# Optimization experiments

Measured on AMD Instinct MI355X. Metric: run time of the kernel, lower is better.

Reference implementation:

```python
import jax, jax.numpy as jnp
import numpy as np

H, C = 3, 64  # heads, per-head channels
NEG_SLOPE = 0.2

def setup_inputs() -> dict:
    key = jax.random.key(0)
    ks = jax.random.split(key, 8)
    B, N, D, E = 2, 50000, 128, 800000
    h = jax.random.normal(ks[0], (B, N, D), dtype=jnp.float32)
    edge_index = jax.random.randint(ks[1], (2, E), 0, N, dtype=jnp.int64)
    s = 1.0 / np.sqrt(D)
    W = jax.random.normal(ks[2], (D, H * C), dtype=jnp.float32) * s
    a_src = jax.random.normal(ks[3], (H, C), dtype=jnp.float32) * (1.0 / np.sqrt(C))
    a_dst = jax.random.normal(ks[4], (H, C), dtype=jnp.float32) * (1.0 / np.sqrt(C))
    bias = jnp.zeros((H * C,), dtype=jnp.float32)
    Wo = jax.random.normal(ks[5], (H * C, 1), dtype=jnp.float32) * (1.0 / np.sqrt(H * C))
    bo = jnp.zeros((1,), dtype=jnp.float32)
    return {"h": h, "edge_index": edge_index, "W": W, "a_src": a_src,
            "a_dst": a_dst, "bias": bias, "Wo": Wo, "bo": bo}

def _gat_single(h_b, src, dst, N, W, a_src, a_dst, bias):
    # h_b: [N, D] -> x: [N, H, C]
    x = (h_b @ W).reshape(-1, H, C)
    alpha_s = jnp.einsum('nhc,hc->nh', x, a_src)  # [N, H]
    alpha_d = jnp.einsum('nhc,hc->nh', x, a_dst)  # [N, H]
    e = alpha_s[src] + alpha_d[dst]               # [E', H]
    e = jnp.where(e > 0, e, NEG_SLOPE * e)        # leaky_relu(0.2)
    # segment softmax over edges grouped by destination node
    emax = jax.ops.segment_max(e, dst, num_segments=N)          # [N, H]
    p = jnp.exp(e - emax[dst])
    denom = jax.ops.segment_sum(p, dst, num_segments=N)         # [N, H]
    att = p / (denom[dst] + 1e-16)                               # [E', H]
    out = jax.ops.segment_sum(att[:, :, None] * x[src], dst, num_segments=N)  # [N,H,C]
    return out.reshape(-1, H * C) + bias

def reference(h, edge_index, W, a_src, a_dst, bias, Wo, bo):
    B, N, D = h.shape
    # PyG GATConv default: add self loops
    loops = jnp.arange(N, dtype=edge_index.dtype)
    src = jnp.concatenate([edge_index[0], loops])
    dst = jnp.concatenate([edge_index[1], loops])
    gat = jax.vmap(lambda hb: _gat_single(hb, src, dst, N, W, a_src, a_dst, bias))(h)
    gat = jax.nn.elu(gat)            # [B, N, H*C]; dropout inactive (eval)
    logits = gat @ Wo + bo           # [B, N, 1]
    return logits
```

## Files before the change

kernel.cpp:

```cpp
#include <hip/hip_runtime.h>
#include <hip/hip_bf16.h>
#include <math.h>

typedef __hip_bfloat16 bf16;
typedef __attribute__((ext_vector_type(8))) short short8;
typedef __attribute__((ext_vector_type(4))) short short4v;
typedef __attribute__((ext_vector_type(4))) float f32x4;

#define HC 192
#define DIN 128
#define NEG_SLOPE 0.2f
#define GN 4
#define CAP 56
#define GROWS 128

static inline int cdiv(int a, int b){ return (a + b - 1) / b; }

__device__ inline short f2bf(float f){
  __hip_bfloat16 b = __float2bfloat16(f);
  return __builtin_bit_cast(short, b);
}
__device__ inline float loadf(const void* p, size_t i, int fm){
  return fm ? __bfloat162float(((const bf16*)p)[i]) : ((const float*)p)[i];
}
__device__ inline int eload(const void* p, long long i, int em){
  return em ? (int)(((const long long*)p)[i]) : ((const int*)p)[i];
}

__device__ inline int detect_fm(const unsigned* __restrict__ hw){
  unsigned w = hw[threadIdx.x & 63];
  unsigned expo = (w >> 7) & 0xFF;
  unsigned long long m = __ballot(expo >= 100 && expo <= 135);
  return __popcll(m) > 32;
}
__device__ inline int detect_em(const unsigned* __restrict__ ew){
  unsigned long long m = __ballot(ew[2*(threadIdx.x & 63) + 1] != 0);
  return __popcll(m) < 32;
}

__global__ void k_repack(const void* __restrict__ W, const void* __restrict__ a_src,
    const void* __restrict__ a_dst, const void* __restrict__ bias,
    const void* __restrict__ Wo, const void* __restrict__ bo,
    const unsigned* __restrict__ hw, bf16* __restrict__ Wt,
    float* __restrict__ asf, float* __restrict__ adf, float* __restrict__ biasf,
    float* __restrict__ Wof, float* __restrict__ bof,
    int* __restrict__ counts, int N){
  int fm = detect_fm(hw);
  int idx = blockIdx.x * 256 + threadIdx.x;
  for (int i = idx; i < N; i += 96 * 256) counts[i] = 0;
  if (idx < DIN * HC){
    int d = idx / HC, j = idx - d * HC;
    Wt[j * DIN + d] = __float2bfloat16(loadf(W, idx, fm));
  }
  if (idx < HC){
    asf[idx]   = loadf(a_src, idx, fm);
    adf[idx]   = loadf(a_dst, idx, fm);
    biasf[idx] = loadf(bias, idx, fm);
    Wof[idx]   = loadf(Wo, idx, fm);
  }
  if (idx == 0) bof[0] = loadf(bo, 0, fm);
}

__global__ __launch_bounds__(512) void k_fused(const void* __restrict__ h,
    const bf16* __restrict__ Wt, bf16* __restrict__ x,
    const float* __restrict__ asf, const float* __restrict__ adf,
    float* __restrict__ asp, float* __restrict__ adp,
    const void* __restrict__ ei, int* __restrict__ counts,
    unsigned* __restrict__ srcs, int M, int N, int E, int NBG){
  __shared__ short ldsW[HC * 136];

  if ((int)blockIdx.x >= NBG){
    int em = detect_em((const unsigned*)ei);
    int idx = ((int)blockIdx.x - NBG) * 512 + (int)threadIdx.x;
    if (idx >= E + N) return;
    int s, d;
    if (idx < E){
      s = eload(ei, idx, em);
      d = eload(ei, (long long)E + idx, em);
    } else { s = d = idx - E; }
    if ((unsigned)d >= (unsigned)N) return;
    if ((unsigned)s >= (unsigned)N) s = 0;
    int slot = atomicAdd(&counts[d], 1);
    if (slot >= CAP) return;
    srcs[(size_t)d * CAP + slot] = (unsigned)s;
    return;
  }

  int fm   = detect_fm((const unsigned*)h);
  int tid  = threadIdx.x;
  int w    = tid >> 6;
  int lane = tid & 63;
  int r16  = lane & 15;
  int quad = lane >> 4;
  for (int c = tid; c < HC * 16; c += 512){
    int row = c >> 4, kg = c & 15;
    *(short8*)&ldsW[row * 136 + kg * 8] = *(const short8*)(Wt + row * DIN + kg * 8);
  }
  __syncthreads();

  int row  = (int)blockIdx.x * GROWS + w * 16 + r16;
  int lrow = min(row, M - 1);
  f32x4 acc[12];
  #pragma unroll
  for (int i = 0; i < 12; i++) acc[i] = (f32x4){0.f,0.f,0.f,0.f};
  size_t hbase = (size_t)lrow * DIN + quad * 8;
  #pragma unroll
  for (int kb = 0; kb < 4; kb++){
    short8 bh;
    if (fm == 0){
      const float* hf = (const float*)h + hbase + kb * 32;
      float4 a = *(const float4*)hf;
      float4 b = *(const float4*)(hf + 4);
      bh[0]=f2bf(a.x); bh[1]=f2bf(a.y); bh[2]=f2bf(a.z); bh[3]=f2bf(a.w);
      bh[4]=f2bf(b.x); bh[5]=f2bf(b.y); bh[6]=f2bf(b.z); bh[7]=f2bf(b.w);
    } else {
      bh = *(const short8*)((const bf16*)h + hbase + kb * 32);
    }
    #pragma unroll
    for (int nt = 0; nt < 12; nt++){
      short8 aw = *(const short8*)&ldsW[(nt*16 + r16) * 136 + kb * 32 + quad * 8];
      acc[nt] = __builtin_amdgcn_mfma_f32_16x16x32_bf16(aw, bh, acc[nt], 0,0,0);
    }
  }
  if (row < M){
    int bb    = row >= N;
    int nodeR = row - bb * N;
    bf16* xr  = x + ((size_t)nodeR * 2 + bb) * HC;
    #pragma unroll
    for (int nt = 0; nt < 12; nt++){
      short4v pk = { f2bf(acc[nt][0]), f2bf(acc[nt][1]),
                     f2bf(acc[nt][2]), f2bf(acc[nt][3]) };
      *(short4v*)(xr + nt*16 + quad*4) = pk;
    }
  }
  float vs[3] = {0.f,0.f,0.f}, vd[3] = {0.f,0.f,0.f};
  #pragma unroll
  for (int nt = 0; nt < 12; nt++){
    int hh = nt >> 2;
    f32x4 a4 = *(const f32x4*)(asf + nt*16 + quad*4);
    f32x4 d4 = *(const f32x4*)(adf + nt*16 + quad*4);
    vs[hh] += acc[nt][0]*a4[0] + acc[nt][1]*a4[1] + acc[nt][2]*a4[2] + acc[nt][3]*a4[3];
    vd[hh] += acc[nt][0]*d4[0] + acc[nt][1]*d4[1] + acc[nt][2]*d4[2] + acc[nt][3]*d4[3];
  }
  #pragma unroll
  for (int hh = 0; hh < 3; hh++){
    float v1 = vs[hh], v2 = vd[hh];
    v1 += __shfl_down(v1, 32);  v1 += __shfl_down(v1, 16);
    v2 += __shfl_down(v2, 32);  v2 += __shfl_down(v2, 16);
    if (lane < 16 && row < M){
      int b = row >= N;
      int node = row - b * N;
      asp[(size_t)node*8 + b*3 + hh] = v1;
      adp[(size_t)node*8 + b*3 + hh] = v2;
    }
  }
}

__global__ __launch_bounds__(192) void k_gat(const bf16* __restrict__ x,
    const unsigned* __restrict__ srcs, const int* __restrict__ cnt,
    const float* __restrict__ asp, const float* __restrict__ adp,
    const float* __restrict__ biasf, const float* __restrict__ Wof,
    const float* __restrict__ bof, float* __restrict__ out, int N){
  int blk  = blockIdx.x;
  int t    = threadIdx.x;
  int node = t / 48;
  int u    = t - node * 48;
  int b    = u >= 24;
  int c8   = u - b * 24;
  int hh   = c8 >> 3;
  __shared__ int      cs[GN];
  __shared__ float    adl[GN * 6];
  __shared__ unsigned ldsS[GN * CAP];
  __shared__ float    ldsP[GN * CAP * 6];
  __shared__ float    red[192];
  if (t < GN) cs[t] = min(cnt[GN*blk + t], CAP);
  if (t < GN * 6){
    int nd = t / 6, k = t - nd * 6;
    adl[t] = adp[(size_t)(GN*blk + nd) * 8 + k];
  }
  __syncthreads();
  for (int j = t; j < GN * CAP; j += 192){
    int nd = j / CAP, sl = j - nd * CAP;
    if (sl < cs[nd]) ldsS[j] = srcs[(size_t)(GN*blk + nd) * CAP + sl];
  }
  __syncthreads();
  for (int j = t; j < GN * CAP; j += 192){
    int nd = j / CAP, sl = j - nd * CAP;
    if (sl < cs[nd]){
      int s = (int)ldsS[j];
      float4 A0 = *(const float4*)(asp + (size_t)s * 8);
      float4 A1 = *(const float4*)(asp + (size_t)s * 8 + 4);
      float e0 = A0.x + adl[nd*6+0], e1 = A0.y + adl[nd*6+1];
      float e2 = A0.z + adl[nd*6+2], e3 = A0.w + adl[nd*6+3];
      float e4 = A1.x + adl[nd*6+4], e5 = A1.y + adl[nd*6+5];
      e0 = e0 > 0.f ? e0 : NEG_SLOPE*e0;  e1 = e1 > 0.f ? e1 : NEG_SLOPE*e1;
      e2 = e2 > 0.f ? e2 : NEG_SLOPE*e2;  e3 = e3 > 0.f ? e3 : NEG_SLOPE*e3;
      e4 = e4 > 0.f ? e4 : NEG_SLOPE*e4;  e5 = e5 > 0.f ? e5 : NEG_SLOPE*e5;
      ldsP[j*6 + 0] = __expf(e0);  ldsP[j*6 + 1] = __expf(e1);
      ldsP[j*6 + 2] = __expf(e2);  ldsP[j*6 + 3] = __expf(e3);
      ldsP[j*6 + 4] = __expf(e4);  ldsP[j*6 + 5] = __expf(e5);
    }
  }
  __syncthreads();
  int mycnt = cs[node];
  int pidx  = b*3 + hh;
  const ushort* xb = (const ushort*)x + (size_t)b * HC + c8 * 8;
  float acc[8];
  #pragma unroll
  for (int k = 0; k < 8; k++) acc[k] = 0.f;
  float den = 0.f;
  int rbase = node * CAP;
  #pragma unroll 8
  for (int i = 0; i < mycnt; i++){
    int rec = rbase + i;
    float p = ldsP[rec*6 + pidx];
    int s   = (int)ldsS[rec];
    uint4 q = *(const uint4*)(xb + (size_t)s * (2 * HC));
    den += p;
    acc[0] = fmaf(p, __uint_as_float(q.x << 16),         acc[0]);
    acc[1] = fmaf(p, __uint_as_float(q.x & 0xffff0000u), acc[1]);
    acc[2] = fmaf(p, __uint_as_float(q.y << 16),         acc[2]);
    acc[3] = fmaf(p, __uint_as_float(q.y & 0xffff0000u), acc[3]);
    acc[4] = fmaf(p, __uint_as_float(q.z << 16),         acc[4]);
    acc[5] = fmaf(p, __uint_as_float(q.z & 0xffff0000u), acc[5]);
    acc[6] = fmaf(p, __uint_as_float(q.w << 16),         acc[6]);
    acc[7] = fmaf(p, __uint_as_float(q.w & 0xffff0000u), acc[7]);
  }
  float inv = 1.f / (den + 1e-16f);
  float4 bi0 = ((const float4*)biasf)[c8*2], bi1 = ((const float4*)biasf)[c8*2+1];
  float4 w0  = ((const float4*)Wof)[c8*2],  w1  = ((const float4*)Wof)[c8*2+1];
  float r = 0.f;
  {
    float v;
    v = acc[0]*inv + bi0.x; v = v > 0.f ? v : expm1f(v); r += v * w0.x;
    v = acc[1]*inv + bi0.y; v = v > 0.f ? v : expm1f(v); r += v * w0.y;
    v = acc[2]*inv + bi0.z; v = v > 0.f ? v : expm1f(v); r += v * w0.z;
    v = acc[3]*inv + bi0.w; v = v > 0.f ? v : expm1f(v); r += v * w0.w;
    v = acc[4]*inv + bi1.x; v = v > 0.f ? v : expm1f(v); r += v * w1.x;
    v = acc[5]*inv + bi1.y; v = v > 0.f ? v : expm1f(v); r += v * w1.y;
    v = acc[6]*inv + bi1.z; v = v > 0.f ? v : expm1f(v); r += v * w1.z;
    v = acc[7]*inv + bi1.w; v = v > 0.f ? v : expm1f(v); r += v * w1.w;
  }
  red[t] = r;
  __syncthreads();
  if (t < 64){
    int g = t >> 3, l = t & 7;
    float v = red[g*24 + l] + red[g*24 + 8 + l] + red[g*24 + 16 + l];
    v += __shfl_down(v, 4, 8);
    v += __shfl_down(v, 2, 8);
    v += __shfl_down(v, 1, 8);
    if (l == 0){
      int nd = GN*blk + (g >> 1);
      int bb = g & 1;
      out[(size_t)bb * N + nd] = v + bof[0];
    }
  }
}

extern "C" void kernel_launch(void* const* d_in, const int* in_sizes, int n_in,
                              void* d_out, int out_size, void* d_ws, size_t ws_size,
                              hipStream_t stream){
  const void* h     = d_in[0];
  const void* ei    = d_in[1];
  const void* W     = d_in[2];
  const void* a_src = d_in[3];
  const void* a_dst = d_in[4];
  const void* bias  = d_in[5];
  const void* Wo    = d_in[6];
  const void* bo    = d_in[7];
  float* out = (float*)d_out;

  const int M    = in_sizes[0] / DIN;
  const int N    = M / 2;
  const int E    = in_sizes[1] / 2;
  const int Etot = E + N;

  char* ws = (char*)d_ws;
  size_t off = 0;
  auto alloc = [&](size_t bytes) -> void* {
    void* p = ws + off;
    off = (off + bytes + 511) & ~(size_t)511;
    return p;
  };
  bf16*     x      = (bf16*)    alloc((size_t)M * HC * sizeof(bf16));
  float*    asp    = (float*)   alloc((size_t)N * 8 * sizeof(float));
  float*    adp    = (float*)   alloc((size_t)N * 8 * sizeof(float));
  int*      counts = (int*)     alloc((size_t)N * sizeof(int));
  unsigned* srcs   = (unsigned*)alloc((size_t)N * CAP * sizeof(unsigned));
  bf16*     Wt     = (bf16*)    alloc((size_t)DIN * HC * sizeof(bf16));
  float*    asf    = (float*)   alloc(HC * sizeof(float));
  float*    adf    = (float*)   alloc(HC * sizeof(float));
  float*    biasf  = (float*)   alloc(HC * sizeof(float));
  float*    Wof    = (float*)   alloc(HC * sizeof(float));
  float*    bof    = (float*)   alloc(16 * sizeof(float));
  (void)ws_size; (void)n_in; (void)out_size;

  const int NBG = cdiv(M, GROWS);
  const int NBB = cdiv(Etot, 512);

  k_repack<<<96, 256, 0, stream>>>(W, a_src, a_dst, bias, Wo, bo,
      (const unsigned*)h, Wt, asf, adf, biasf, Wof, bof, counts, N);
  k_fused<<<NBG + NBB, 512, 0, stream>>>(h, Wt, x, asf, adf, asp, adp,
      ei, counts, srcs, M, N, E, NBG);
  k_gat<<<N / GN, 192, 0, stream>>>(x, srcs, counts, asp, adp,
      biasf, Wof, bof, out, N);
}
```

Before: 265.3 us.

## Fold weight repack into fused GEMM and restructure GAT aggregation per-wave

Removes the separate repack kernel. Each GEMM block now converts and transposes W into LDS itself, and a_src/a_dst, bias, Wo and bo are loaded into shared memory inside the consuming kernels. The aggregation kernel now handles 8 nodes per 512-thread block with one wave per node, merges the src-loading and exp passes, and uses a 3-deep register prefetch of gathered rows plus a shuffle-only reduction. In exchange, every GEMM block redundantly reads W from global memory with strided scalar loads, and the gather kernel's LDS and occupancy profile changes.

```diff
diff --git a/kernel.cpp b/kernel.cpp
--- a/kernel.cpp
+++ b/kernel.cpp
@@ -6,11 +6,12 @@
 typedef __attribute__((ext_vector_type(8))) short short8;
 typedef __attribute__((ext_vector_type(4))) short short4v;
 typedef __attribute__((ext_vector_type(4))) float f32x4;
+typedef __attribute__((ext_vector_type(2))) float f32x2;
 
 #define HC 192
 #define DIN 128
 #define NEG_SLOPE 0.2f
-#define GN 4
+#define GN 8
 #define CAP 56
 #define GROWS 128
 
@@ -38,36 +39,20 @@
   return __popcll(m) < 32;
 }
 
-__global__ void k_repack(const void* __restrict__ W, const void* __restrict__ a_src,
-    const void* __restrict__ a_dst, const void* __restrict__ bias,
-    const void* __restrict__ Wo, const void* __restrict__ bo,
-    const unsigned* __restrict__ hw, bf16* __restrict__ Wt,
-    float* __restrict__ asf, float* __restrict__ adf, float* __restrict__ biasf,
-    float* __restrict__ Wof, float* __restrict__ bof,
-    int* __restrict__ counts, int N){
-  int fm = detect_fm(hw);
+__global__ void k_zero(int* __restrict__ counts, int N){
   int idx = blockIdx.x * 256 + threadIdx.x;
   for (int i = idx; i < N; i += 96 * 256) counts[i] = 0;
-  if (idx < DIN * HC){
-    int d = idx / HC, j = idx - d * HC;
-    Wt[j * DIN + d] = __float2bfloat16(loadf(W, idx, fm));
-  }
-  if (idx < HC){
-    asf[idx]   = loadf(a_src, idx, fm);
-    adf[idx]   = loadf(a_dst, idx, fm);
-    biasf[idx] = loadf(bias, idx, fm);
-    Wof[idx]   = loadf(Wo, idx, fm);
-  }
-  if (idx == 0) bof[0] = loadf(bo, 0, fm);
 }
 
 __global__ __launch_bounds__(512) void k_fused(const void* __restrict__ h,
-    const bf16* __restrict__ Wt, bf16* __restrict__ x,
-    const float* __restrict__ asf, const float* __restrict__ adf,
+    const void* __restrict__ W, const void* __restrict__ a_src,
+    const void* __restrict__ a_dst, bf16* __restrict__ x,
     float* __restrict__ asp, float* __restrict__ adp,
     const void* __restrict__ ei, int* __restrict__ counts,
     unsigned* __restrict__ srcs, int M, int N, int E, int NBG){
-  __shared__ short ldsW[HC * 136];
+  __shared__ alignas(16) short ldsW[HC * 136];
+  __shared__ alignas(16) float asfL[HC];
+  __shared__ alignas(16) float adfL[HC];
 
   if ((int)blockIdx.x >= NBG){
     int em = detect_em((const unsigned*)ei);
@@ -92,9 +77,15 @@
   int lane = tid & 63;
   int r16  = lane & 15;
   int quad = lane >> 4;
-  for (int c = tid; c < HC * 16; c += 512){
-    int row = c >> 4, kg = c & 15;
-    *(short8*)&ldsW[row * 136 + kg * 8] = *(const short8*)(Wt + row * DIN + kg * 8);
+  if (tid < HC)           asfL[tid]        = loadf(a_src, tid, fm);
+  else if (tid < 2 * HC)  adfL[tid - HC]   = loadf(a_dst, tid - HC, fm);
+  for (int pi = tid; pi < HC * 16; pi += 512){
+    int j = pi % HC, dblk = pi / HC;
+    short8 v8;
+    #pragma unroll
+    for (int kk = 0; kk < 8; kk++)
+      v8[kk] = f2bf(loadf(W, (size_t)(dblk * 8 + kk) * HC + j, fm));
+    *(short8*)&ldsW[j * 136 + dblk * 8] = v8;
   }
   __syncthreads();
 
@@ -137,8 +128,8 @@
   #pragma unroll
   for (int nt = 0; nt < 12; nt++){
     int hh = nt >> 2;
-    f32x4 a4 = *(const f32x4*)(asf + nt*16 + quad*4);
-    f32x4 d4 = *(const f32x4*)(adf + nt*16 + quad*4);
+    f32x4 a4 = *(const f32x4*)&asfL[nt*16 + quad*4];
+    f32x4 d4 = *(const f32x4*)&adfL[nt*16 + quad*4];
     vs[hh] += acc[nt][0]*a4[0] + acc[nt][1]*a4[1] + acc[nt][2]*a4[2] + acc[nt][3]*a4[3];
     vd[hh] += acc[nt][0]*d4[0] + acc[nt][1]*d4[1] + acc[nt][2]*d4[2] + acc[nt][3]*d4[3];
   }
@@ -156,38 +147,40 @@
   }
 }
 
-__global__ __launch_bounds__(192) void k_gat(const bf16* __restrict__ x,
+__global__ __launch_bounds__(512) void k_gat(const bf16* __restrict__ x,
     const unsigned* __restrict__ srcs, const int* __restrict__ cnt,
     const float* __restrict__ asp, const float* __restrict__ adp,
-    const float* __restrict__ biasf, const float* __restrict__ Wof,
-    const float* __restrict__ bof, float* __restrict__ out, int N){
+    const void* __restrict__ bias, const void* __restrict__ Wo,
+    const void* __restrict__ bo, const unsigned* __restrict__ hw,
+    float* __restrict__ out, int N){
+  int fm   = detect_fm(hw);
   int blk  = blockIdx.x;
   int t    = threadIdx.x;
-  int node = t / 48;
-  int u    = t - node * 48;
-  int b    = u >= 24;
-  int c8   = u - b * 24;
-  int hh   = c8 >> 3;
-  __shared__ int      cs[GN];
+  __shared__ int      csL[GN];
   __shared__ float    adl[GN * 6];
   __shared__ unsigned ldsS[GN * CAP];
   __shared__ float    ldsP[GN * CAP * 6];
-  __shared__ float    red[192];
-  if (t < GN) cs[t] = min(cnt[GN*blk + t], CAP);
+  __shared__ alignas(16) float biasL[HC];
+  __shared__ alignas(16) float WoL[HC];
+  __shared__ float    boL;
+  if (t < HC)           biasL[t]      = loadf(bias, t, fm);
+  else if (t < 2 * HC)  WoL[t - HC]   = loadf(Wo, t - HC, fm);
+  else if (t == 511)    boL           = loadf(bo, 0, fm);
+  if (t < GN){
+    int nd = GN*blk + t;
+    csL[t] = (nd < N) ? min(cnt[nd], CAP) : 0;
+  }
   if (t < GN * 6){
     int nd = t / 6, k = t - nd * 6;
-    adl[t] = adp[(size_t)(GN*blk + nd) * 8 + k];
+    int nodeid = GN*blk + nd;
+    adl[t] = (nodeid < N) ? adp[(size_t)nodeid * 8 + k] : 0.f;
   }
   __syncthreads();
-  for (int j = t; j < GN * CAP; j += 192){
-    int nd = j / CAP, sl = j - nd * CAP;
-    if (sl < cs[nd]) ldsS[j] = srcs[(size_t)(GN*blk + nd) * CAP + sl];
-  }
-  __syncthreads();
-  for (int j = t; j < GN * CAP; j += 192){
-    int nd = j / CAP, sl = j - nd * CAP;
-    if (sl < cs[nd]){
-      int s = (int)ldsS[j];
+  if (t < GN * CAP){
+    int nd = t / CAP, sl = t - nd * CAP;
+    if (sl < csL[nd]){
+      int s = (int)srcs[(size_t)(GN*blk + nd) * CAP + sl];
+      ldsS[t] = (unsigned)s;
       float4 A0 = *(const float4*)(asp + (size_t)s * 8);
       float4 A1 = *(const float4*)(asp + (size_t)s * 8 + 4);
       float e0 = A0.x + adl[nd*6+0], e1 = A0.y + adl[nd*6+1];
@@ -196,65 +189,81 @@
       e0 = e0 > 0.f ? e0 : NEG_SLOPE*e0;  e1 = e1 > 0.f ? e1 : NEG_SLOPE*e1;
       e2 = e2 > 0.f ? e2 : NEG_SLOPE*e2;  e3 = e3 > 0.f ? e3 : NEG_SLOPE*e3;
       e4 = e4 > 0.f ? e4 : NEG_SLOPE*e4;  e5 = e5 > 0.f ? e5 : NEG_SLOPE*e5;
-      ldsP[j*6 + 0] = __expf(e0);  ldsP[j*6 + 1] = __expf(e1);
-      ldsP[j*6 + 2] = __expf(e2);  ldsP[j*6 + 3] = __expf(e3);
-      ldsP[j*6 + 4] = __expf(e4);  ldsP[j*6 + 5] = __expf(e5);
+      ldsP[t*6 + 0] = __expf(e0);  ldsP[t*6 + 1] = __expf(e1);
+      ldsP[t*6 + 2] = __expf(e2);  ldsP[t*6 + 3] = __expf(e3);
+      ldsP[t*6 + 4] = __expf(e4);  ldsP[t*6 + 5] = __expf(e5);
     }
   }
   __syncthreads();
-  int mycnt = cs[node];
-  int pidx  = b*3 + hh;
-  const ushort* xb = (const ushort*)x + (size_t)b * HC + c8 * 8;
-  float acc[8];
-  #pragma unroll
-  for (int k = 0; k < 8; k++) acc[k] = 0.f;
-  float den = 0.f;
-  int rbase = node * CAP;
-  #pragma unroll 8
-  for (int i = 0; i < mycnt; i++){
-    int rec = rbase + i;
-    float p = ldsP[rec*6 + pidx];
-    int s   = (int)ldsS[rec];
-    uint4 q = *(const uint4*)(xb + (size_t)s * (2 * HC));
-    den += p;
-    acc[0] = fmaf(p, __uint_as_float(q.x << 16),         acc[0]);
-    acc[1] = fmaf(p, __uint_as_float(q.x & 0xffff0000u), acc[1]);
-    acc[2] = fmaf(p, __uint_as_float(q.y << 16),         acc[2]);
-    acc[3] = fmaf(p, __uint_as_float(q.y & 0xffff0000u), acc[3]);
-    acc[4] = fmaf(p, __uint_as_float(q.z << 16),         acc[4]);
-    acc[5] = fmaf(p, __uint_as_float(q.z & 0xffff0000u), acc[5]);
-    acc[6] = fmaf(p, __uint_as_float(q.w << 16),         acc[6]);
-    acc[7] = fmaf(p, __uint_as_float(q.w & 0xffff0000u), acc[7]);
-  }
-  float inv = 1.f / (den + 1e-16f);
-  float4 bi0 = ((const float4*)biasf)[c8*2], bi1 = ((const float4*)biasf)[c8*2+1];
-  float4 w0  = ((const float4*)Wof)[c8*2],  w1  = ((const float4*)Wof)[c8*2+1];
-  float r = 0.f;
-  {
-    float v;
-    v = acc[0]*inv + bi0.x; v = v > 0.f ? v : expm1f(v); r += v * w0.x;
-    v = acc[1]*inv + bi0.y; v = v > 0.f ? v : expm1f(v); r += v * w0.y;
-    v = acc[2]*inv + bi0.z; v = v > 0.f ? v : expm1f(v); r += v * w0.z;
-    v = acc[3]*inv + bi0.w; v = v > 0.f ? v : expm1f(v); r += v * w0.w;
-    v = acc[4]*inv + bi1.x; v = v > 0.f ? v : expm1f(v); r += v * w1.x;
-    v = acc[5]*inv + bi1.y; v = v > 0.f ? v : expm1f(v); r += v * w1.y;
-    v = acc[6]*inv + bi1.z; v = v > 0.f ? v : expm1f(v); r += v * w1.z;
-    v = acc[7]*inv + bi1.w; v = v > 0.f ? v : expm1f(v); r += v * w1.w;
-  }
-  red[t] = r;
-  __syncthreads();
-  if (t < 64){
-    int g = t >> 3, l = t & 7;
-    float v = red[g*24 + l] + red[g*24 + 8 + l] + red[g*24 + 16 + l];
-    v += __shfl_down(v, 4, 8);
-    v += __shfl_down(v, 2, 8);
-    v += __shfl_down(v, 1, 8);
-    if (l == 0){
-      int nd = GN*blk + (g >> 1);
-      int bb = g & 1;
-      out[(size_t)bb * N + nd] = v + bof[0];
-    }
-  }
+
+  int w    = t >> 6;
+  int lane = t & 63;
+  int node = GN*blk + w;
+  float r  = 0.f;
+  if (node < N){
+    int b     = lane & 1;
+    int c8    = lane >> 1;
+    int mycnt = csL[w];
+    int rbase = w * CAP;
+    if (c8 < 24){
+      int hh   = c8 >> 3;
+      int pidx = b*3 + hh;
+      const ushort* xb = (const ushort*)x + b * HC + c8 * 8;
+      f32x2 a0 = {0.f,0.f}, a1 = {0.f,0.f}, a2 = {0.f,0.f}, a3 = {0.f,0.f};
+      float den = 0.f;
+      auto LD = [&](int i) -> uint4 {
+        int s = (int)ldsS[rbase + i];
+        return *(const uint4*)(xb + (size_t)s * (2 * HC));
+      };
+      auto PROC = [&](int i, uint4 q){
+        float p = ldsP[(rbase + i)*6 + pidx];
+        den += p;
+        f32x2 pp = {p, p};
+        f32x2 v;
+        v[0] = __uint_as_float(q.x << 16); v[1] = __uint_as_float(q.x & 0xffff0000u);
+        a0 += pp * v;
+        v[0] = __uint_as_float(q.y << 16); v[1] = __uint_as_float(q.y & 0xffff0000u);
+        a1 += pp * v;
+        v[0] = __uint_as_float(q.z << 16); v[1] = __uint_as_float(q.z & 0xffff0000u);
+        a2 += pp * v;
+        v[0] = __uint_as_float(q.w << 16); v[1] = __uint_as_float(q.w & 0xffff0000u);
+        a3 += pp * v;
+      };
+      uint4 q0 = {}, q1 = {}, q2 = {};
+      if (mycnt > 0) q0 = LD(0);
+      if (mycnt > 1) q1 = LD(1);
+      if (mycnt > 2) q2 = LD(2);
+      int i = 0;
+      for (; i + 3 <= mycnt; i += 3){
+        PROC(i,     q0); if (i + 3 < mycnt) q0 = LD(i + 3);
+        PROC(i + 1, q1); if (i + 4 < mycnt) q1 = LD(i + 4);
+        PROC(i + 2, q2); if (i + 5 < mycnt) q2 = LD(i + 5);
+      }
+      if (i     < mycnt) PROC(i,     q0);
+      if (i + 1 < mycnt) PROC(i + 1, q1);
+      float inv = 1.f / (den + 1e-16f);
+      f32x4 bi0 = *(const f32x4*)&biasL[c8*8];
+      f32x4 bi1 = *(const f32x4*)&biasL[c8*8 + 4];
+      f32x4 w0  = *(const f32x4*)&WoL[c8*8];
+      f32x4 w1  = *(const f32x4*)&WoL[c8*8 + 4];
+      float v;
+      v = a0[0]*inv + bi0[0]; v = v > 0.f ? v : expm1f(v); r += v * w0[0];
+      v = a0[1]*inv + bi0[1]; v = v > 0.f ? v : expm1f(v); r += v * w0[1];
+      v = a1[0]*inv + bi0[2]; v = v > 0.f ? v : expm1f(v); r += v * w0[2];
+      v = a1[1]*inv + bi0[3]; v = v > 0.f ? v : expm1f(v); r += v * w0[3];
+      v = a2[0]*inv + bi1[0]; v = v > 0.f ? v : expm1f(v); r += v * w1[0];
+      v = a2[1]*inv + bi1[1]; v = v > 0.f ? v : expm1f(v); r += v * w1[1];
+      v = a3[0]*inv + bi1[2]; v = v > 0.f ? v : expm1f(v); r += v * w1[2];
+      v = a3[1]*inv + bi1[3]; v = v > 0.f ? v : expm1f(v); r += v * w1[3];
+    }
+  }
+  r += __shfl_xor(r, 2);
+  r += __shfl_xor(r, 4);
+  r += __shfl_xor(r, 8);
+  r += __shfl_xor(r, 16);
+  r += __shfl_xor(r, 32);
+  if (lane < 2 && node < N)
+    out[(size_t)lane * N + node] = r + boL;
 }
 
 extern "C" void kernel_launch(void* const* d_in, const int* in_sizes, int n_in,
@@ -287,21 +296,14 @@
   float*    adp    = (float*)   alloc((size_t)N * 8 * sizeof(float));
   int*      counts = (int*)     alloc((size_t)N * sizeof(int));
   unsigned* srcs   = (unsigned*)alloc((size_t)N * CAP * sizeof(unsigned));
-  bf16*     Wt     = (bf16*)    alloc((size_t)DIN * HC * sizeof(bf16));
-  float*    asf    = (float*)   alloc(HC * sizeof(float));
-  float*    adf    = (float*)   alloc(HC * sizeof(float));
-  float*    biasf  = (float*)   alloc(HC * sizeof(float));
-  float*    Wof    = (float*)   alloc(HC * sizeof(float));
-  float*    bof    = (float*)   alloc(16 * sizeof(float));
   (void)ws_size; (void)n_in; (void)out_size;
 
   const int NBG = cdiv(M, GROWS);
   const int NBB = cdiv(Etot, 512);
 
-  k_repack<<<96, 256, 0, stream>>>(W, a_src, a_dst, bias, Wo, bo,
-      (const unsigned*)h, Wt, asf, adf, biasf, Wof, bof, counts, N);
-  k_fused<<<NBG + NBB, 512, 0, stream>>>(h, Wt, x, asf, adf, asp, adp,
+  k_zero<<<96, 256, 0, stream>>>(counts, N);
+  k_fused<<<NBG + NBB, 512, 0, stream>>>(h, W, a_src, a_dst, x, asp, adp,
       ei, counts, srcs, M, N, E, NBG);
-  k_gat<<<N / GN, 192, 0, stream>>>(x, srcs, counts, asp, adp,
-      biasf, Wof, bof, out, N);
-}
+  k_gat<<<cdiv(N, GN), 512, 0, stream>>>(x, srcs, counts, asp, adp,
+      bias, Wo, bo, (const unsigned*)h, out, N);
+}
```

New measurement: 266.2 us. Within noise of the previous version (+0.4%).
